# Kernel tuning notes

Hardware: AMD Instinct MI355X
Metric: run time of the kernel (lower is better)

Reference implementation:

```python
import jax, jax.numpy as jnp
import numpy as np

HIDDEN = 2048
NUM_HEADS = 16
HEAD_DIM = 128
ROPE_BASE = 10000.0
B, L = 2, 2048


def _rotate_half(x):
    x1, x2 = jnp.split(x, 2, axis=-1)
    return jnp.concatenate((-x2, x1), axis=-1)


def _apply_rope(x, position_ids, base=ROPE_BASE):
    # x: [B, L, H, D]; position_ids: [L] (broadcast over batch)
    D = x.shape[-1]
    dim_idx = jnp.arange(0, D, 2, dtype=jnp.float32)
    inv_freq = 1.0 / (base ** (dim_idx / D))                      # [D/2]
    freqs = position_ids.astype(jnp.float32)[None, :, None] * inv_freq  # [1, L, D/2]
    # NOTE: faithful to source: sin/cos are repeat_interleaved ([s0,s0,s1,s1,...])
    sin = jnp.repeat(jnp.sin(freqs), 2, axis=-1)[:, :, None, :]   # [1, L, 1, D]
    cos = jnp.repeat(jnp.cos(freqs), 2, axis=-1)[:, :, None, :]
    return cos * x + _rotate_half(x) * sin


def setup_inputs() -> dict:
    key = jax.random.key(0)
    k1, k2, k3, k4, k5 = jax.random.split(key, 5)
    hidden_states = jax.random.normal(k1, (B, L, HIDDEN), dtype=jnp.float32)
    # causal additive mask, broadcastable over heads
    causal = jnp.tril(jnp.ones((L, L), dtype=bool))
    attention_mask = jnp.where(causal, 0.0, -1e9).astype(jnp.float32)
    attention_mask = jnp.broadcast_to(attention_mask, (B, 1, L, L))
    position_ids = jnp.arange(L, dtype=jnp.int64)
    s = 1.0 / np.sqrt(HIDDEN)
    Wq = jax.random.normal(k2, (HIDDEN, NUM_HEADS * HEAD_DIM), dtype=jnp.float32) * s
    Wk = jax.random.normal(k3, (HIDDEN, NUM_HEADS * HEAD_DIM), dtype=jnp.float32) * s
    Wv = jax.random.normal(k4, (HIDDEN, NUM_HEADS * HEAD_DIM), dtype=jnp.float32) * s
    Wo = jax.random.normal(k5, (NUM_HEADS * HEAD_DIM, HIDDEN), dtype=jnp.float32) * s
    return {"hidden_states": hidden_states, "attention_mask": attention_mask,
            "position_ids": position_ids, "Wq": Wq, "Wk": Wk, "Wv": Wv, "Wo": Wo}


def reference(hidden_states, attention_mask, position_ids, Wq, Wk, Wv, Wo):
    Bb, Ll, _ = hidden_states.shape
    H, D = NUM_HEADS, HEAD_DIM
    scale = D ** -0.5
    q = (hidden_states @ Wq).reshape(Bb, Ll, H, D)
    k = (hidden_states @ Wk).reshape(Bb, Ll, H, D)
    v = (hidden_states @ Wv).reshape(Bb, Ll, H, D)
    q = _apply_rope(q, position_ids)
    k = _apply_rope(k, position_ids)
    # [B, H, Lq, Lk]
    scores = jnp.einsum('bqhd,bkhd->bhqk', q, k) * scale + attention_mask
    attn = jax.nn.softmax(scores.astype(jnp.float32), axis=-1).astype(q.dtype)
    out = jnp.einsum('bhqk,bkhd->bqhd', attn, v).reshape(Bb, Ll, H * D)
    return out @ Wo
```

## Files before the change

### kernel.cpp

```cpp
#include <hip/hip_runtime.h>
#include <stdint.h>

typedef uint16_t u16;
typedef __attribute__((ext_vector_type(4))) float f32x4;
typedef __attribute__((ext_vector_type(2))) unsigned short u16x2;
typedef __attribute__((ext_vector_type(4))) unsigned short u16x4;
typedef __attribute__((ext_vector_type(8))) __bf16 bf16x8;

#define HIDDEN 2048
#define LSEQ   2048
#define NH     16
#define HD     128
#define NQK    6144
#define QSCALE 0.12751743f
#define M0 32.0f

__device__ __forceinline__ u16 f2b(float f) {
  union { float f; uint32_t u; } v; v.f = f;
  uint32_t r = v.u + 0x7fffu + ((v.u >> 16) & 1u);
  return (u16)(r >> 16);
}
__device__ __forceinline__ float b2f(u16 h) {
  union { uint32_t u; float f; } v; v.u = ((uint32_t)h) << 16;
  return v.f;
}

__device__ __forceinline__ void gload16(const void* g, void* l) {
  __builtin_amdgcn_global_load_lds((const __attribute__((address_space(1))) void*)g,
                                   (__attribute__((address_space(3))) void*)l, 16, 0, 0);
}
__device__ __forceinline__ f32x4 mfma16(bf16x8 a, bf16x8 b, f32x4 c) {
  return __builtin_amdgcn_mfma_f32_16x16x32_bf16(a, b, c, 0, 0, 0);
}

__global__ void k_f32_to_bf16(const float* __restrict__ in, u16* __restrict__ out, int n4) {
  int i = blockIdx.x * 256 + threadIdx.x;
  if (i >= n4) return;
  float4 v = ((const float4*)in)[i];
  u16x4 o = { f2b(v.x), f2b(v.y), f2b(v.z), f2b(v.w) };
  ((u16x4*)out)[i] = o;
}

__global__ __launch_bounds__(256) void k_prep(const float* __restrict__ Wq,
                                              const float* __restrict__ Wk,
                                              const float* __restrict__ Wv,
                                              const float* __restrict__ Wo,
                                              u16* __restrict__ WT, u16* __restrict__ WoT,
                                              const int* __restrict__ pos, int pstride,
                                              float* __restrict__ tab) {
  const int z = blockIdx.z;
  if (z == 4) {
    int i = (blockIdx.y * 32 + blockIdx.x) * 256 + threadIdx.x;
    if (i >= LSEQ * 64) return;
    int l = i >> 6, j = i & 63;
    float p = (float)pos[(size_t)l * pstride];
    float th = p * expf(-(float)j * 0.14391156642178528f);
    tab[2 * i + 0] = cosf(th);
    tab[2 * i + 1] = sinf(th);
    return;
  }
  const float* W = (z == 0) ? Wq : (z == 1) ? Wk : (z == 2) ? Wv : Wo;
  u16* D = (z < 3) ? (WT + (size_t)z * HIDDEN * HIDDEN) : WoT;
  const float scale = (z == 0) ? QSCALE : 1.0f;
  const int R = HIDDEN, C = HIDDEN;

  __shared__ u16 tile[64][65];
  const int bx = blockIdx.x, by = blockIdx.y;
  const int t = threadIdx.x;
  const int g = t >> 4, k = t & 15;
#pragma unroll
  for (int p = 0; p < 4; ++p) {
    int r = by * 64 + p * 16 + g;
    int c = bx * 64 + k * 4;
    float4 v = *(const float4*)(W + (size_t)r * C + c);
    tile[p * 16 + g][k * 4 + 0] = f2b(v.x * scale);
    tile[p * 16 + g][k * 4 + 1] = f2b(v.y * scale);
    tile[p * 16 + g][k * 4 + 2] = f2b(v.z * scale);
    tile[p * 16 + g][k * 4 + 3] = f2b(v.w * scale);
  }
  __syncthreads();
#pragma unroll
  for (int p = 0; p < 4; ++p) {
    int n = bx * 64 + p * 16 + g;
    int kk = by * 64 + k * 4;
    u16x4 o = { tile[k * 4 + 0][p * 16 + g], tile[k * 4 + 1][p * 16 + g],
                tile[k * 4 + 2][p * 16 + g], tile[k * 4 + 3][p * 16 + g] };
    *(u16x4*)(D + (size_t)n * R + kk) = o;
  }
}

__global__ void k_rope_apply(u16* __restrict__ qkv, const float* __restrict__ tab) {
  int i = blockIdx.x * 256 + threadIdx.x;
  int dph = i & 31;
  int h = (i >> 5) & 15;
  int mat = (i >> 9) & 1;
  int row = i >> 10;
  int l = row & (LSEQ - 1);
  const float* t1 = tab + 2 * (l * 64 + dph);
  const float* t2 = tab + 2 * (l * 64 + 32 + dph);
  size_t base = (size_t)row * NQK + mat * HIDDEN + h * HD + dph * 2;
  u16x2 xa = *(u16x2*)(qkv + base);
  u16x2 xb = *(u16x2*)(qkv + base + 64);
  float x1a = b2f(xa[0]), x1b = b2f(xa[1]), x2a = b2f(xb[0]), x2b = b2f(xb[1]);
  u16x2 oa = { f2b(t1[0] * x1a - t1[1] * x2a), f2b(t1[0] * x1b - t1[1] * x2b) };
  u16x2 ob = { f2b(t2[0] * x2a + t2[1] * x1a), f2b(t2[0] * x2b + t2[1] * x1b) };
  *(u16x2*)(qkv + base) = oa;
  *(u16x2*)(qkv + base + 64) = ob;
}

__global__ __launch_bounds__(256) void k_transpose_v(const u16* __restrict__ qkv,
                                                     u16* __restrict__ vt) {
  __shared__ u16 tile[64][65];
  const int lt = blockIdx.x;
  const int dt = blockIdx.y;
  const int bh = blockIdx.z;
  const int t = threadIdx.x;
  const int g = t >> 4, k = t & 15;
  const u16* src = qkv + (size_t)(bh >> 4) * LSEQ * NQK + 2 * HIDDEN + (bh & 15) * HD;
#pragma unroll
  for (int p = 0; p < 4; ++p) {
    int l = lt * 64 + p * 16 + g;
    int d = dt * 64 + k * 4;
    u16x4 v = *(const u16x4*)(src + (size_t)l * NQK + d);
    tile[p * 16 + g][k * 4 + 0] = v[0];
    tile[p * 16 + g][k * 4 + 1] = v[1];
    tile[p * 16 + g][k * 4 + 2] = v[2];
    tile[p * 16 + g][k * 4 + 3] = v[3];
  }
  __syncthreads();
  u16* dst = vt + (size_t)bh * HD * LSEQ;
#pragma unroll
  for (int p = 0; p < 4; ++p) {
    int d = dt * 64 + p * 16 + g;
    int l = lt * 64 + k * 4;
    u16x4 o = { tile[k * 4 + 0][p * 16 + g], tile[k * 4 + 1][p * 16 + g],
                tile[k * 4 + 2][p * 16 + g], tile[k * 4 + 3][p * 16 + g] };
    *(u16x4*)(dst + (size_t)d * LSEQ + l) = o;
  }
}

template<int BF16OUT>
__global__ __launch_bounds__(512, 2) void k_gemm2(const u16* __restrict__ A,
                                                  const u16* __restrict__ Bt,
                                                  void* __restrict__ Cv,
                                                  int M, int N, int K) {
  __shared__ __align__(16) char lds[147456];
  const int tid = threadIdx.x, w = tid >> 6, lane = tid & 63;
  const int l15 = lane & 15, l4 = lane >> 4;
  const int wm = w >> 2, wn = w & 3;
  const int nbx = gridDim.x;
  const int nwg = nbx * gridDim.y;
  const int id = blockIdx.y * nbx + blockIdx.x;
  const int qq = nwg >> 3;
  const int sid = (id & 7) * qq + (id >> 3);
  const int bn = sid % nbx, bm = sid / nbx;
  const u16* Ag = A + (size_t)bm * 128 * K;
  const u16* Bg = Bt + (size_t)bn * 256 * K;
  const int r7 = (tid >> 3) & 7;
  const int sw0 = ((0 + l4) ^ (l15 & 7)) * 16;
  const int sw1 = ((4 + l4) ^ (l15 & 7)) * 16;

  auto stageA = [&](int kt, int buf) {
    char* dst = lds + buf * 16384;
    const int k0 = kt << 6;
#pragma unroll
    for (int i = 0; i < 2; ++i) {
      int c = i * 512 + tid;
      int row = c >> 3, s = (c & 7) ^ r7;
      gload16(Ag + (size_t)row * K + k0 + s * 8, dst + (i * 512 + w * 64) * 16);
    }
  };
  auto stageBh = [&](int kt, int buf, int half) {
    char* dst = lds + 49152 + buf * 32768;
    const int k0 = kt << 6;
#pragma unroll
    for (int i = 0; i < 2; ++i) {
      int c = half * 1024 + i * 512 + tid;
      int row = c >> 3, s = (c & 7) ^ r7;
      gload16(Bg + (size_t)row * K + k0 + s * 8, dst + (half * 1024 + i * 512 + w * 64) * 16);
    }
  };

  const int NT = K >> 6;
  stageA(0, 0); stageBh(0, 0, 0); stageBh(0, 0, 1);
  stageA(1, 1); stageBh(1, 1, 0); stageBh(1, 1, 1);
  asm volatile("s_waitcnt vmcnt(6)" ::: "memory");
  __builtin_amdgcn_s_barrier();
  asm volatile("" ::: "memory");

  f32x4 acc[4][4] = {};
  int buf = 0, sbuf = 2;
  for (int t = 0; t < NT; ++t) {
    const char* Ab = lds + buf * 16384;
    const char* Bb = lds + 49152 + buf * 32768;
    const bool doStage = (t + 2 < NT);
    bf16x8 af[4][2], bfr[4][2];
    auto rdA = [&](int mi, int ks) {
      return *(const bf16x8*)(Ab + ((wm * 64 + mi * 16 + l15) << 7) + (ks ? sw1 : sw0));
    };
    auto rdB = [&](int nj, int ks) {
      return *(const bf16x8*)(Bb + ((wn * 64 + nj * 16 + l15) << 7) + (ks ? sw1 : sw0));
    };

#pragma unroll
    for (int mi = 0; mi < 2; ++mi) { af[mi][0] = rdA(mi, 0); af[mi][1] = rdA(mi, 1); }
#pragma unroll
    for (int nj = 0; nj < 2; ++nj) { bfr[nj][0] = rdB(nj, 0); bfr[nj][1] = rdB(nj, 1); }
    if (doStage) stageA(t + 2, sbuf);
    __builtin_amdgcn_s_setprio(1);
#pragma unroll
    for (int mi = 0; mi < 2; ++mi)
#pragma unroll
      for (int nj = 0; nj < 2; ++nj) {
        acc[mi][nj] = mfma16(af[mi][0], bfr[nj][0], acc[mi][nj]);
        acc[mi][nj] = mfma16(af[mi][1], bfr[nj][1], acc[mi][nj]);
      }
    __builtin_amdgcn_s_setprio(0);

#pragma unroll
    for (int nj = 2; nj < 4; ++nj) { bfr[nj][0] = rdB(nj, 0); bfr[nj][1] = rdB(nj, 1); }
    if (doStage) stageBh(t + 2, sbuf, 0);
    __builtin_amdgcn_s_setprio(1);
#pragma unroll
    for (int mi = 0; mi < 2; ++mi)
#pragma unroll
      for (int nj = 2; nj < 4; ++nj) {
        acc[mi][nj] = mfma16(af[mi][0], bfr[nj][0], acc[mi][nj]);
        acc[mi][nj] = mfma16(af[mi][1], bfr[nj][1], acc[mi][nj]);
      }
    __builtin_amdgcn_s_setprio(0);

#pragma unroll
    for (int mi = 2; mi < 4; ++mi) { af[mi][0] = rdA(mi, 0); af[mi][1] = rdA(mi, 1); }
    if (doStage) stageBh(t + 2, sbuf, 1);
    __builtin_amdgcn_s_setprio(1);
#pragma unroll
    for (int mi = 2; mi < 4; ++mi)
#pragma unroll
      for (int nj = 2; nj < 4; ++nj) {
        acc[mi][nj] = mfma16(af[mi][0], bfr[nj][0], acc[mi][nj]);
        acc[mi][nj] = mfma16(af[mi][1], bfr[nj][1], acc[mi][nj]);
      }
    __builtin_amdgcn_s_setprio(0);

    __builtin_amdgcn_s_setprio(1);
#pragma unroll
    for (int mi = 2; mi < 4; ++mi)
#pragma unroll
      for (int nj = 0; nj < 2; ++nj) {
        acc[mi][nj] = mfma16(af[mi][0], bfr[nj][0], acc[mi][nj]);
        acc[mi][nj] = mfma16(af[mi][1], bfr[nj][1], acc[mi][nj]);
      }
    __builtin_amdgcn_s_setprio(0);

    if (doStage) asm volatile("s_waitcnt vmcnt(6)" ::: "memory");
    else         asm volatile("s_waitcnt vmcnt(0)" ::: "memory");
    __builtin_amdgcn_s_barrier();
    asm volatile("" ::: "memory");
    buf = (buf == 2) ? 0 : buf + 1;
    sbuf = (sbuf == 2) ? 0 : sbuf + 1;
  }

#pragma unroll
  for (int mi = 0; mi < 4; ++mi) {
#pragma unroll
    for (int nj = 0; nj < 4; ++nj) {
      int row0 = bm * 128 + wm * 64 + mi * 16 + l4 * 4;
      int col  = bn * 256 + wn * 64 + nj * 16 + l15;
#pragma unroll
      for (int r = 0; r < 4; ++r) {
        float v = acc[mi][nj][r];
        if (BF16OUT) ((u16*)Cv)[(size_t)(row0 + r) * N + col] = f2b(v);
        else         ((float*)Cv)[(size_t)(row0 + r) * N + col] = v;
      }
    }
  }
}

__global__ __launch_bounds__(512, 2) void k_attn(const u16* __restrict__ qkv,
                                                 const u16* __restrict__ vt,
                                                 u16* __restrict__ aout) {
  __shared__ __align__(16) u16 Ks[3][64 * 128];
  __shared__ __align__(16) u16 Vs[3][128 * 64];
  __shared__ __align__(16) u16 Ps[2][8 * 16 * 72];
  const int bid = blockIdx.x;
  const int bh = bid & 31, pairi = bid >> 5;
  const int b = bh >> 4, h = bh & 15;
  const int qtA = pairi, qtB = 15 - pairi;
  const int tid = threadIdx.x, w = tid >> 6, lane = tid & 63;
  const int l15 = lane & 15, l4 = lane >> 4;

  bf16x8 qfA[4], qfB[4];
  {
    const u16* qpA = qkv + (size_t)(b * LSEQ + qtA * 128 + w * 16 + l15) * NQK + h * HD;
    const u16* qpB = qkv + (size_t)(b * LSEQ + qtB * 128 + w * 16 + l15) * NQK + h * HD;
#pragma unroll
    for (int ks = 0; ks < 4; ++ks) {
      qfA[ks] = *(const bf16x8*)(qpA + ks * 32 + l4 * 8);
      qfB[ks] = *(const bf16x8*)(qpB + ks * 32 + l4 * 8);
    }
  }

  f32x4 accA[8] = {}, accB[8] = {};
  float mA[4], lA[4], mB[4], lB[4];
#pragma unroll
  for (int r = 0; r < 4; ++r) { mA[r] = M0; lA[r] = 0.f; mB[r] = M0; lB[r] = 0.f; }

  const u16* kb  = qkv + (size_t)b * LSEQ * NQK + HIDDEN + h * HD;
  const u16* vtb = vt + (size_t)bh * HD * LSEQ;
  const int ntA = 2 * qtA + 2, ntB = 2 * qtB + 2;
  const int qbaseA = qtA * 128 + w * 16, qbaseB = qtB * 128 + w * 16;

  auto stage = [&](int t, int bf) {
    const int kv0 = t * 64;
    char* Kd = (char*)(&Ks[bf][0]);
    char* Vd = (char*)(&Vs[bf][0]);
#pragma unroll
    for (int p = 0; p < 2; ++p) {
      int cc = p * 512 + tid;
      int row = cc >> 4, sl = cc & 15;
      gload16(kb + (size_t)(kv0 + row) * NQK + ((sl ^ (row & 7)) * 8), Kd + (p * 512 + w * 64) * 16);
    }
#pragma unroll
    for (int p = 0; p < 2; ++p) {
      int cc = p * 512 + tid;
      int d = cc >> 3, sl = cc & 7;
      gload16(vtb + (size_t)d * LSEQ + kv0 + ((sl ^ (d & 7)) * 8), Vd + (p * 512 + w * 64) * 16);
    }
  };

  auto tileCompute = [&](const bf16x8 (&qf)[4], f32x4 (&acc_o)[8], float (&mrun)[4],
                         float (&lrun)[4], int qbase, int kv0,
                         const char* KsC, const char* VsC, u16* ps) {
    f32x4 s4[4] = {};
    __builtin_amdgcn_s_setprio(1);
#pragma unroll
    for (int ks = 0; ks < 4; ++ks) {
#pragma unroll
      for (int nj = 0; nj < 4; ++nj) {
        int row = nj * 16 + l15;
        int co = (ks * 64 + l4 * 16) ^ ((row & 7) << 4);
        bf16x8 kf = *(const bf16x8*)(KsC + row * 256 + co);
        s4[nj] = mfma16(qf[ks], kf, s4[nj]);
      }
    }
    __builtin_amdgcn_s_setprio(0);

    const int qrow0 = qbase + l4 * 4;
    float pv[4][4], lm[4];
    if (kv0 + 63 <= qbase) {
#pragma unroll
      for (int r = 0; r < 4; ++r) {
        lm[r] = fmaxf(fmaxf(s4[0][r], s4[1][r]), fmaxf(s4[2][r], s4[3][r]));
#pragma unroll
        for (int nj = 0; nj < 4; ++nj) pv[nj][r] = s4[nj][r];
      }
    } else {
#pragma unroll
      for (int r = 0; r < 4; ++r) {
        float mx = -3e38f;
#pragma unroll
        for (int nj = 0; nj < 4; ++nj) {
          int kvcol = kv0 + nj * 16 + l15;
          float sv = (kvcol <= qrow0 + r) ? s4[nj][r] : -3e38f;
          pv[nj][r] = sv;
          mx = fmaxf(mx, sv);
        }
        lm[r] = mx;
      }
    }
    int over = (lm[0] > mrun[0]) | (lm[1] > mrun[1]) | (lm[2] > mrun[2]) | (lm[3] > mrun[3]);
    if (__builtin_expect(__any(over), 0)) {
#pragma unroll
      for (int r = 0; r < 4; ++r) {
        float px = lm[r];
        px = fmaxf(px, __shfl_xor(px, 1));
        px = fmaxf(px, __shfl_xor(px, 2));
        px = fmaxf(px, __shfl_xor(px, 4));
        px = fmaxf(px, __shfl_xor(px, 8));
        if (px > mrun[r]) {
          float cf = exp2f(mrun[r] - px);
          mrun[r] = px;
          lrun[r] *= cf;
#pragma unroll
          for (int df = 0; df < 8; ++df) acc_o[df][r] *= cf;
        }
      }
    }
#pragma unroll
    for (int r = 0; r < 4; ++r) {
      float s = 0.f;
#pragma unroll
      for (int nj = 0; nj < 4; ++nj) {
        float e = exp2f(pv[nj][r] - mrun[r]);
        pv[nj][r] = e;
        s += e;
      }
      lrun[r] += s;
    }
#pragma unroll
    for (int nj = 0; nj < 4; ++nj)
#pragma unroll
      for (int r = 0; r < 4; ++r)
        ps[(w * 16 + l4 * 4 + r) * 72 + nj * 16 + l15] = f2b(pv[nj][r]);

    bf16x8 pa[2];
#pragma unroll
    for (int ks2 = 0; ks2 < 2; ++ks2)
      pa[ks2] = *(const bf16x8*)(ps + (w * 16 + l15) * 72 + ks2 * 32 + l4 * 8);
    __builtin_amdgcn_s_setprio(1);
#pragma unroll
    for (int df = 0; df < 8; ++df) {
#pragma unroll
      for (int ks2 = 0; ks2 < 2; ++ks2) {
        int vrow = df * 16 + l15;
        int co = (ks2 * 64 + l4 * 16) ^ ((vrow & 7) << 4);
        bf16x8 bv = *(const bf16x8*)(VsC + vrow * 128 + co);
        acc_o[df] = mfma16(pa[ks2], bv, acc_o[df]);
      }
    }
    __builtin_amdgcn_s_setprio(0);
  };

  stage(0, 0);
  stage(1, 1);
  asm volatile("s_waitcnt vmcnt(4)" ::: "memory");
  __builtin_amdgcn_s_barrier();

  int buf = 0, sbuf = 2;
  for (int t = 0; t < ntB; ++t) {
    const bool doStage = (t + 2 < ntB);
    if (doStage) stage(t + 2, sbuf);
    const int kv0 = t * 64;
    const char* KsC = (const char*)(&Ks[buf][0]);
    const char* VsC = (const char*)(&Vs[buf][0]);

    if ((t < ntA) && (kv0 <= qbaseA + 15))
      tileCompute(qfA, accA, mA, lA, qbaseA, kv0, KsC, VsC, &Ps[0][0]);
    if (kv0 <= qbaseB + 15)
      tileCompute(qfB, accB, mB, lB, qbaseB, kv0, KsC, VsC, &Ps[1][0]);

    if (doStage) asm volatile("s_waitcnt vmcnt(4)" ::: "memory");
    else         asm volatile("s_waitcnt vmcnt(0)" ::: "memory");
    __builtin_amdgcn_s_barrier();
    buf = (buf == 2) ? 0 : buf + 1;
    sbuf = (sbuf == 2) ? 0 : sbuf + 1;
  }

#pragma unroll
  for (int r = 0; r < 4; ++r) {
    float sA = lA[r];
    sA += __shfl_xor(sA, 1); sA += __shfl_xor(sA, 2);
    sA += __shfl_xor(sA, 4); sA += __shfl_xor(sA, 8);
    float sB = lB[r];
    sB += __shfl_xor(sB, 1); sB += __shfl_xor(sB, 2);
    sB += __shfl_xor(sB, 4); sB += __shfl_xor(sB, 8);
    float invA = 1.f / sA;
    float invB = 1.f / sB;
    u16* opA = aout + (size_t)(b * LSEQ + qtA * 128 + w * 16 + l4 * 4 + r) * HIDDEN + h * HD;
    u16* opB = aout + (size_t)(b * LSEQ + qtB * 128 + w * 16 + l4 * 4 + r) * HIDDEN + h * HD;
#pragma unroll
    for (int df = 0; df < 8; ++df) {
      opA[df * 16 + l15] = f2b(accA[df][r] * invA);
      opB[df * 16 + l15] = f2b(accB[df][r] * invB);
    }
  }
}

extern "C" void kernel_launch(void* const* d_in, const int* in_sizes, int n_in,
                              void* d_out, int out_size, void* d_ws, size_t ws_size,
                              hipStream_t stream) {
  const float* hidden = (const float*)d_in[0];
  const int*   pos = (const int*)d_in[2];
  const float* Wq = (const float*)d_in[3];
  const float* Wk = (const float*)d_in[4];
  const float* Wv = (const float*)d_in[5];
  const float* Wo = (const float*)d_in[6];
  float* out = (float*)d_out;

  char* ws = (char*)d_ws;
  u16* hbf   = (u16*)ws;
  u16* WT    = (u16*)(ws + 16777216);
  u16* vt    = WT;
  u16* WoT   = (u16*)(ws + 16777216 + 25165824);
  u16* qkv   = (u16*)(ws + 50331648);
  float* tab = (float*)(ws + 100663296);
  u16* aout  = hbf;

  int pstride = (in_sizes[2] == LSEQ) ? 1 : 2;

  k_f32_to_bf16<<<8192, 256, 0, stream>>>(hidden, hbf, 2097152);
  k_prep<<<dim3(32, 32, 5), 256, 0, stream>>>(Wq, Wk, Wv, Wo, WT, WoT, pos, pstride, tab);
  k_gemm2<1><<<dim3(24, 32), 512, 0, stream>>>(hbf, WT, qkv, 4096, 6144, 2048);
  k_rope_apply<<<16384, 256, 0, stream>>>(qkv, tab);
  k_transpose_v<<<dim3(32, 2, 32), 256, 0, stream>>>(qkv, vt);
  k_attn<<<256, 512, 0, stream>>>(qkv, vt, aout);
  k_gemm2<0><<<dim3(8, 32), 512, 0, stream>>>(aout, WoT, out, 4096, 2048, 2048);
}
```

Baseline: 271.0 us.

## Use 128-wide KV tiles with double buffering in attention kernel

Each staged K/V tile now covers 128 keys instead of 64, and the ring changes from three buffers to two. Every stage is processed as two 64-key sub-tiles, with an offset added to the V reads. The two query tiles now share a single P scratch buffer. This halves the number of barriers and loop iterations per block. The cost is a shallower prefetch: only one tile is in flight, and the kernel fully drains outstanding loads with vmcnt(0) each iteration, which may expose more memory latency.

```diff
diff --git a/kernel.cpp b/kernel.cpp
--- a/kernel.cpp
+++ b/kernel.cpp
@@ -280,9 +280,9 @@
 __global__ __launch_bounds__(512, 2) void k_attn(const u16* __restrict__ qkv,
                                                  const u16* __restrict__ vt,
                                                  u16* __restrict__ aout) {
-  __shared__ __align__(16) u16 Ks[3][64 * 128];
-  __shared__ __align__(16) u16 Vs[3][128 * 64];
-  __shared__ __align__(16) u16 Ps[2][8 * 16 * 72];
+  __shared__ __align__(16) u16 Ks[2][128 * 128];
+  __shared__ __align__(16) u16 Vs[2][128 * 128];
+  __shared__ __align__(16) u16 Ps[8 * 16 * 72];
   const int bid = blockIdx.x;
   const int bh = bid & 31, pairi = bid >> 5;
   const int b = bh >> 4, h = bh & 15;
@@ -308,30 +308,30 @@
 
   const u16* kb  = qkv + (size_t)b * LSEQ * NQK + HIDDEN + h * HD;
   const u16* vtb = vt + (size_t)bh * HD * LSEQ;
-  const int ntA = 2 * qtA + 2, ntB = 2 * qtB + 2;
+  const int nt = qtB + 1;
   const int qbaseA = qtA * 128 + w * 16, qbaseB = qtB * 128 + w * 16;
 
   auto stage = [&](int t, int bf) {
-    const int kv0 = t * 64;
+    const int kv0 = t * 128;
     char* Kd = (char*)(&Ks[bf][0]);
     char* Vd = (char*)(&Vs[bf][0]);
 #pragma unroll
-    for (int p = 0; p < 2; ++p) {
+    for (int p = 0; p < 4; ++p) {
       int cc = p * 512 + tid;
       int row = cc >> 4, sl = cc & 15;
       gload16(kb + (size_t)(kv0 + row) * NQK + ((sl ^ (row & 7)) * 8), Kd + (p * 512 + w * 64) * 16);
     }
 #pragma unroll
-    for (int p = 0; p < 2; ++p) {
+    for (int p = 0; p < 4; ++p) {
       int cc = p * 512 + tid;
-      int d = cc >> 3, sl = cc & 7;
+      int d = cc >> 4, sl = cc & 15;
       gload16(vtb + (size_t)d * LSEQ + kv0 + ((sl ^ (d & 7)) * 8), Vd + (p * 512 + w * 64) * 16);
     }
   };
 
   auto tileCompute = [&](const bf16x8 (&qf)[4], f32x4 (&acc_o)[8], float (&mrun)[4],
                          float (&lrun)[4], int qbase, int kv0,
-                         const char* KsC, const char* VsC, u16* ps) {
+                         const char* KsC, const char* VsC, int voff, u16* ps) {
     f32x4 s4[4] = {};
     __builtin_amdgcn_s_setprio(1);
 #pragma unroll
@@ -415,7 +415,7 @@
       for (int ks2 = 0; ks2 < 2; ++ks2) {
         int vrow = df * 16 + l15;
         int co = (ks2 * 64 + l4 * 16) ^ ((vrow & 7) << 4);
-        bf16x8 bv = *(const bf16x8*)(VsC + vrow * 128 + co);
+        bf16x8 bv = *(const bf16x8*)(VsC + vrow * 256 + (co + voff));
         acc_o[df] = mfma16(pa[ks2], bv, acc_o[df]);
       }
     }
@@ -423,28 +423,25 @@
   };
 
   stage(0, 0);
-  stage(1, 1);
-  asm volatile("s_waitcnt vmcnt(4)" ::: "memory");
+  asm volatile("s_waitcnt vmcnt(0)" ::: "memory");
   __builtin_amdgcn_s_barrier();
 
-  int buf = 0, sbuf = 2;
-  for (int t = 0; t < ntB; ++t) {
-    const bool doStage = (t + 2 < ntB);
-    if (doStage) stage(t + 2, sbuf);
-    const int kv0 = t * 64;
-    const char* KsC = (const char*)(&Ks[buf][0]);
-    const char* VsC = (const char*)(&Vs[buf][0]);
-
-    if ((t < ntA) && (kv0 <= qbaseA + 15))
-      tileCompute(qfA, accA, mA, lA, qbaseA, kv0, KsC, VsC, &Ps[0][0]);
-    if (kv0 <= qbaseB + 15)
-      tileCompute(qfB, accB, mB, lB, qbaseB, kv0, KsC, VsC, &Ps[1][0]);
-
-    if (doStage) asm volatile("s_waitcnt vmcnt(4)" ::: "memory");
-    else         asm volatile("s_waitcnt vmcnt(0)" ::: "memory");
+  for (int t = 0; t < nt; ++t) {
+    const int bf = t & 1;
+    if (t + 1 < nt) stage(t + 1, bf ^ 1);
+    const char* KsC = (const char*)(&Ks[bf][0]);
+    const char* VsC = (const char*)(&Vs[bf][0]);
+#pragma unroll
+    for (int sub = 0; sub < 2; ++sub) {
+      const int kv0 = t * 128 + sub * 64;
+      const char* Ksub = KsC + sub * 16384;
+      if (kv0 <= qbaseA + 15)
+        tileCompute(qfA, accA, mA, lA, qbaseA, kv0, Ksub, VsC, sub * 128, &Ps[0]);
+      if (kv0 <= qbaseB + 15)
+        tileCompute(qfB, accB, mB, lB, qbaseB, kv0, Ksub, VsC, sub * 128, &Ps[0]);
+    }
+    asm volatile("s_waitcnt vmcnt(0)" ::: "memory");
     __builtin_amdgcn_s_barrier();
-    buf = (buf == 2) ? 0 : buf + 1;
-    sbuf = (sbuf == 2) ? 0 : sbuf + 1;
   }
 
 #pragma unroll
```

Result: slower. 459.7 us (+69.6%).
